# Kernel tuning notes

Hardware: AMD Instinct MI355X
Metric: run time of the kernel (lower is better)

The kernel has to match this reference:

```python
import jax, jax.numpy as jnp
import numpy as np

XY, Z, NT = 10, 5, 10000
S = XY * XY * Z  # 500 states
NEG = np.float32(-1e9)  # finite stand-in for log(0); exp(NEG - m) == 0 in fp32


def _build_log_transitions(rng):
    # Reproduce initialize_transitions(): per-row softmax over the 7-neighbor
    # stencil [(0,0,0),(1,0,0),(-1,0,0),(0,1,0),(0,-1,0),(0,0,1),(0,0,2)],
    # zeros (=> log -inf) elsewhere. Vectorized construction.
    s = np.arange(S)
    z, r = np.divmod(s, XY * XY)
    y, x = np.divmod(r, XY)
    coords = np.stack([x, y, z], -1)                      # [S,3]
    offsets = np.array([[0,0,0],[1,0,0],[-1,0,0],[0,1,0],[0,-1,0],[0,0,1],[0,0,2]])
    nb = coords[:, None, :] + offsets[None, :, :]         # [S,7,3]
    valid = ((nb[..., 0] >= 0) & (nb[..., 0] < XY) &
             (nb[..., 1] >= 0) & (nb[..., 1] < XY) &
             (nb[..., 2] >= 0) & (nb[..., 2] < Z))
    dest = nb[..., 0] + XY * (nb[..., 1] + XY * nb[..., 2])  # [S,7]
    mask = np.zeros((S, S), bool)
    rows = np.broadcast_to(s[:, None], (S, 7))
    mask[rows[valid], dest[valid]] = True
    logits = rng.standard_normal((S, S)).astype(np.float32)
    logits = np.where(mask, logits, NEG)
    m = logits.max(-1, keepdims=True)
    lse = m + np.log(np.exp(logits - m).sum(-1, keepdims=True))
    logT = np.where(mask, (logits - lse).astype(np.float32), NEG)
    return jnp.asarray(logT)


def setup_inputs() -> dict:
    key = jax.random.key(0)
    k1, k2, k3 = jax.random.split(key, 3)
    rng = np.random.default_rng(0)
    B, T, L = 32, 40, 20
    log_priors = jax.nn.log_softmax(jax.random.normal(k1, (S,), dtype=jnp.float32))
    log_emissions = jax.nn.log_softmax(
        jax.random.normal(k2, (S, NT), dtype=jnp.float32), axis=-1)
    log_transitions = _build_log_transitions(rng)
    stories_tensor = jax.random.randint(k3, (B, T, L), 0, NT)
    return {
        "log_priors": log_priors,
        "log_transitions": log_transitions,
        "log_emissions": log_emissions,
        "stories_tensor": stories_tensor,
        "story_length": T,
    }


def reference(log_priors, log_transitions, log_emissions, stories_tensor, story_length):
    # Emission log-probs per (story, time): sum token log-probs over sentence.
    # log_emissions.T: [NT, S]; stories_tensor: [B, T, L] -> em: [B, T, S]
    em = jnp.take(log_emissions.T, stories_tensor, axis=0).sum(axis=2)
    alpha0 = em[:, 0] + log_priors  # [B, S]

    def step(alpha, em_t):
        # broadcast-add then logsumexp over source state (last axis)
        new = em_t + jax.nn.logsumexp(
            log_transitions[None, :, :] + alpha[:, None, :], axis=-1)
        return new, new

    _, rest = jax.lax.scan(step, alpha0, jnp.swapaxes(em[:, 1:], 0, 1))
    return jnp.concatenate([alpha0[None], rest], axis=0)  # [T, B, S]
```

## Files before the change

kernel.cpp:

```cpp
#include <hip/hip_runtime.h>

#define S   500
#define B   32
#define T   40
#define L   20
#define NT  10000
#define NEG (-1e9f)

__global__ __launch_bounds__(512) void emission_kernel(
    const float* __restrict__ logE, const int* __restrict__ stories,
    const float* __restrict__ priors, float* __restrict__ out)
{
    __shared__ float2 pair[NT];
    const int s0  = blockIdx.x * 2;
    const int tid = threadIdx.x;

    const float* r0 = logE + (size_t)s0 * NT;
    const float* r1 = r0 + NT;
    for (int i = tid; i < NT; i += 512)
        pair[i] = make_float2(r0[i], r1[i]);
    __syncthreads();

    const float p0 = priors[s0], p1 = priors[s0 + 1];
    for (int p = tid; p < B * T; p += 512) {
        const int4* tk = (const int4*)(stories + p * L);
        float acc0 = 0.f, acc1 = 0.f;
        #pragma unroll
        for (int q = 0; q < L / 4; ++q) {
            const int4 v = tk[q];
            float2 a = pair[v.x], b2 = pair[v.y], c = pair[v.z], d = pair[v.w];
            acc0 += a.x + b2.x + c.x + d.x;
            acc1 += a.y + b2.y + c.y + d.y;
        }
        const int b = p / T, t = p % T;
        if (t == 0) { acc0 += p0; acc1 += p1; }
        *(float2*)(out + ((size_t)t * B + b) * S + s0) = make_float2(acc0, acc1);
    }
}

__global__ __launch_bounds__(512) void forward_kernel(
    const float* __restrict__ logT, float* __restrict__ out)
{
    constexpr int PAD = 16, AN = 768;
    __shared__ float abuf[2][AN];
    const int s = threadIdx.x;
    const int b = blockIdx.x;
    const bool act = (s < S);
    const int i = s + PAD;

    for (int k = s; k < AN; k += 512) { abuf[0][k] = 0.f; abuf[1][k] = 0.f; }

    float tv0 = NEG, tv1 = NEG, tv2 = NEG, tv3 = NEG, tv4 = NEG, tv5 = NEG, tv6 = NEG;
    if (act) {
        const int x = s % 10, y = (s / 10) % 10, z = s / 100;
        const float* rowT = logT + (size_t)s * S;
        tv0 = rowT[s];
        if (x + 1 < 10) tv1 = rowT[s + 1];
        if (x - 1 >= 0) tv2 = rowT[s - 1];
        if (y + 1 < 10) tv3 = rowT[s + 10];
        if (y - 1 >= 0) tv4 = rowT[s - 10];
        if (z + 1 < 5)  tv5 = rowT[s + 100];
        if (z + 2 < 5)  tv6 = rowT[s + 200];
    }

    const size_t base = (size_t)b * S + s;
    float self = 0.f;
    if (act) self = out[base];
    abuf[0][i] = self;

    float em_next = 0.f;
    if (act) em_next = out[(size_t)B * S + base];
    __syncthreads();

    const float* ap = abuf[0];
    float*       an = abuf[1];

    for (int t = 1; t < T; ++t) {
        const float em_t = em_next;
        if (act && t + 1 < T) em_next = out[(size_t)(t + 1) * B * S + base];

        float a = 0.f;
        if (act) {
            const float v0 = tv0 + self;
            const float v1 = tv1 + ap[i + 1];
            const float v2 = tv2 + ap[i - 1];
            const float v3 = tv3 + ap[i + 10];
            const float v4 = tv4 + ap[i - 10];
            const float v5 = tv5 + ap[i + 100];
            const float v6 = tv6 + ap[i + 200];
            float m = fmaxf(fmaxf(fmaxf(v0, v1), fmaxf(v2, v3)),
                            fmaxf(fmaxf(v4, v5), v6));
            float sum = __expf(v0 - m) + __expf(v1 - m) + __expf(v2 - m) +
                        __expf(v3 - m) + __expf(v4 - m) + __expf(v5 - m) +
                        __expf(v6 - m);
            a = em_t + m + __logf(sum);
            out[(size_t)t * B * S + base] = a;
        }
        an[i] = a;
        self = a;
        float* tmp = an; an = (float*)ap; ap = tmp;
        __syncthreads();
    }
}

extern "C" void kernel_launch(void* const* d_in, const int* in_sizes, int n_in,
                              void* d_out, int out_size, void* d_ws, size_t ws_size,
                              hipStream_t stream) {
    const float* priors  = (const float*)d_in[0];
    const float* logT    = (const float*)d_in[1];
    const float* logE    = (const float*)d_in[2];
    const int*   stories = (const int*)d_in[3];
    float* out = (float*)d_out;

    emission_kernel<<<S / 2, 512, 0, stream>>>(logE, stories, priors, out);
    forward_kernel<<<B, 512, 0, stream>>>(logT, out);
}
```

Measured before the change: 99.61 us.

## Use base-2 log-space, lighter barriers, deeper emission prefetch, vectorized emission loads

The forward recurrence now works in log2 units. Transitions and alpha are pre-scaled by 1/ln2 so the logsumexp can use exp2/log2 directly, and results are converted back on store. __syncthreads is replaced by a bare LDS waitcnt plus s_barrier that skips the vmem wait, emissions are prefetched two steps ahead, and the emission staging loop loads float4 rows. The bare barrier relies on the global stores not needing completion before the barrier, and the change of units adds small rounding differences.

```diff
diff --git a/kernel.cpp b/kernel.cpp
--- a/kernel.cpp
+++ b/kernel.cpp
@@ -6,6 +6,8 @@
 #define L   20
 #define NT  10000
 #define NEG (-1e9f)
+#define INV_LN2 1.44269504088896340736f
+#define LN2f    0.69314718055994530942f
 
 __global__ __launch_bounds__(512) void emission_kernel(
     const float* __restrict__ logE, const int* __restrict__ stories,
@@ -15,10 +17,16 @@
     const int s0  = blockIdx.x * 2;
     const int tid = threadIdx.x;
 
-    const float* r0 = logE + (size_t)s0 * NT;
-    const float* r1 = r0 + NT;
-    for (int i = tid; i < NT; i += 512)
-        pair[i] = make_float2(r0[i], r1[i]);
+    const float4* r0 = (const float4*)(logE + (size_t)s0 * NT);
+    const float4* r1 = (const float4*)(logE + (size_t)(s0 + 1) * NT);
+    for (int i = tid; i < NT / 4; i += 512) {
+        const float4 a4 = r0[i], b4 = r1[i];
+        float2* dst = pair + i * 4;
+        dst[0] = make_float2(a4.x, b4.x);
+        dst[1] = make_float2(a4.y, b4.y);
+        dst[2] = make_float2(a4.z, b4.z);
+        dst[3] = make_float2(a4.w, b4.w);
+    }
     __syncthreads();
 
     const float p0 = priors[s0], p1 = priors[s0 + 1];
@@ -62,22 +70,29 @@
         if (z + 1 < 5)  tv5 = rowT[s + 100];
         if (z + 2 < 5)  tv6 = rowT[s + 200];
     }
+    tv0 *= INV_LN2; tv1 *= INV_LN2; tv2 *= INV_LN2; tv3 *= INV_LN2;
+    tv4 *= INV_LN2; tv5 *= INV_LN2; tv6 *= INV_LN2;
 
     const size_t base = (size_t)b * S + s;
     float self = 0.f;
-    if (act) self = out[base];
+    if (act) self = out[base] * INV_LN2;
     abuf[0][i] = self;
 
-    float em_next = 0.f;
-    if (act) em_next = out[(size_t)B * S + base];
-    __syncthreads();
+    float em1 = 0.f, em2 = 0.f;
+    if (act) em1 = out[(size_t)B * S + base];
+    if (act) em2 = out[(size_t)2 * B * S + base];
+
+    __asm__ __volatile__("s_waitcnt lgkmcnt(0)" ::: "memory");
+    __builtin_amdgcn_s_barrier();
+    __asm__ __volatile__("" ::: "memory");
 
     const float* ap = abuf[0];
     float*       an = abuf[1];
 
     for (int t = 1; t < T; ++t) {
-        const float em_t = em_next;
-        if (act && t + 1 < T) em_next = out[(size_t)(t + 1) * B * S + base];
+        const float em_t = em1;
+        em1 = em2;
+        if (act && t + 2 < T) em2 = out[(size_t)(t + 2) * B * S + base];
 
         float a = 0.f;
         if (act) {
@@ -88,18 +103,21 @@
             const float v4 = tv4 + ap[i - 10];
             const float v5 = tv5 + ap[i + 100];
             const float v6 = tv6 + ap[i + 200];
-            float m = fmaxf(fmaxf(fmaxf(v0, v1), fmaxf(v2, v3)),
-                            fmaxf(fmaxf(v4, v5), v6));
-            float sum = __expf(v0 - m) + __expf(v1 - m) + __expf(v2 - m) +
-                        __expf(v3 - m) + __expf(v4 - m) + __expf(v5 - m) +
-                        __expf(v6 - m);
-            a = em_t + m + __logf(sum);
-            out[(size_t)t * B * S + base] = a;
+            const float m = fmaxf(fmaxf(fmaxf(fmaxf(fmaxf(fmaxf(v0, v1), v2),
+                                                    v3), v4), v5), v6);
+            const float sum = exp2f(v0 - m) + exp2f(v1 - m) + exp2f(v2 - m) +
+                              exp2f(v3 - m) + exp2f(v4 - m) + exp2f(v5 - m) +
+                              exp2f(v6 - m);
+            a = fmaf(em_t, INV_LN2, m + __log2f(sum));
+            out[(size_t)t * B * S + base] = a * LN2f;
         }
         an[i] = a;
         self = a;
         float* tmp = an; an = (float*)ap; ap = tmp;
-        __syncthreads();
+
+        __asm__ __volatile__("s_waitcnt lgkmcnt(0)" ::: "memory");
+        __builtin_amdgcn_s_barrier();
+        __asm__ __volatile__("" ::: "memory");
     }
 }
 
```

Measured after the change: 100.1 us. Within noise of the previous version (+0.5%).
